# Performance work log

Measured on AMD Instinct MI355X. Metric: run time of the kernel, lower is better.

## Reference

```python
import jax, jax.numpy as jnp
import numpy as np

H, W, WS, KS, D, CF, HEAD = 64, 64, 8, 8, 512, 128, 8
INC = D + CF  # 640
GH, GW = H // WS, W // WS  # 8, 8
G = GH * GW  # 64 windows
NW = WS * WS  # 64 tokens per window
DH = D // HEAD  # 64


def _ln(x, g, b, eps=1e-5):
    m = jnp.mean(x, axis=-1, keepdims=True)
    v = jnp.var(x, axis=-1, keepdims=True)
    return (x - m) * jax.lax.rsqrt(v + eps) * g + b


def _lin(x, w, b):
    # torch Linear: w [out,in]
    return jnp.einsum('...i,oi->...o', x, w) + b


def _dwconv(x_nchw, w, b):
    # depthwise conv, stride=KS, VALID; w [C,1,KS,KS]
    y = jax.lax.conv_general_dilated(
        x_nchw, w, window_strides=(KS, KS), padding='VALID',
        feature_group_count=x_nchw.shape[1])
    return y + b[None, :, None, None]


def _win(x):  # [bt,H,W,c] -> [bt,G,NW,c]
    bt, _, _, c = x.shape
    x = x.reshape(bt, GH, WS, GW, WS, c).transpose(0, 1, 3, 2, 4, 5)
    return x.reshape(bt, G, NW, c)


def setup_inputs() -> dict:
    key = jax.random.key(0)
    ks = jax.random.split(key, 20)
    s = 0.02
    inp = {
        'x': jax.random.normal(ks[0], (8, H * W, D), jnp.float32),
        'f': jax.random.normal(ks[1], (8, H * W, CF), jnp.float32),
        'wq': jax.random.normal(ks[2], (D, INC), jnp.float32) * s,
        'bq': jnp.zeros((D,), jnp.float32),
        'wk': jax.random.normal(ks[3], (D, INC), jnp.float32) * s,
        'bk': jnp.zeros((D,), jnp.float32),
        'wv': jax.random.normal(ks[4], (D, D), jnp.float32) * s,
        'bv': jnp.zeros((D,), jnp.float32),
        'wo': jax.random.normal(ks[5], (D, D), jnp.float32) * s,
        'bo': jnp.zeros((D,), jnp.float32),
        'rw_w': jax.random.normal(ks[6], (INC, INC), jnp.float32) * s,
        'rw_b': jnp.zeros((INC,), jnp.float32),
        'convk_w': jax.random.normal(ks[7], (INC, 1, KS, KS), jnp.float32) * s,
        'convk_b': jnp.zeros((INC,), jnp.float32),
        'convv_w': jax.random.normal(ks[8], (D, 1, KS, KS), jnp.float32) * s,
        'convv_b': jnp.zeros((D,), jnp.float32),
        'qn_g': jnp.ones((INC,), jnp.float32), 'qn_b': jnp.zeros((INC,), jnp.float32),
        'kn_g': jnp.ones((INC,), jnp.float32), 'kn_b': jnp.zeros((INC,), jnp.float32),
        'vn_g': jnp.ones((D,), jnp.float32), 'vn_b': jnp.zeros((D,), jnp.float32),
        't': 1,
    }
    return inp


def reference(x, f, wq, bq, wk, bk, wv, bv, wo, bo, rw_w, rw_b,
              convk_w, convk_b, convv_w, convv_b,
              qn_g, qn_b, kn_g, kn_b, vn_g, vn_b, t):
    bt, n, c = x.shape
    x4 = x.reshape(bt, H, W, c)
    f4 = f.reshape(bt, H, W, CF)
    # no padding: H,W divisible by WS
    qk = jnp.concatenate([x4, f4], axis=-1)  # [bt,H,W,INC]
    qk = qk * jax.nn.sigmoid(_lin(qk, rw_w, rw_b))
    q = _win(qk)  # [bt,G,NW,INC]
    # global K tokens via depthwise strided conv
    kg = _dwconv(qk.transpose(0, 3, 1, 2), convk_w, convk_b)  # [bt,INC,GH,GW]
    kg = kg.transpose(0, 2, 3, 1).reshape(bt, 1, -1, INC)
    kg = jnp.broadcast_to(kg, (bt, G, kg.shape[2], INC))
    k = jnp.concatenate([q, kg], axis=2)  # [bt,G,NW+Ng,INC]
    q = _ln(q, qn_g, qn_b)
    k = _ln(k, kn_g, kn_b)
    # global V tokens
    vg = _dwconv(x4.transpose(0, 3, 1, 2), convv_w, convv_b)  # [bt,D,GH,GW]
    vg = vg.transpose(0, 2, 3, 1).reshape(bt, 1, -1, c)
    vg = jnp.broadcast_to(vg, (bt, G, vg.shape[2], c))
    xw = _win(x4)  # [bt,G,NW,c]
    v = _ln(jnp.concatenate([xw, vg], axis=2), vn_g, vn_b)
    # projections
    query = _lin(q, wq, bq).reshape(bt, G, NW, HEAD, DH)
    key = _lin(k, wk, bk).reshape(bt, G, -1, HEAD, DH)
    value = _lin(v, wv, bv).reshape(bt, G, -1, HEAD, DH)
    scores = jnp.einsum('bgqhd,bgkhd->bghqk', query, key) / jnp.sqrt(jnp.float32(DH))
    attn = jax.nn.softmax(scores, axis=-1)
    out = jnp.einsum('bghqk,bgkhd->bgqhd', attn, value).reshape(bt, G, NW, c)
    # window reverse
    out = out.reshape(bt, GH, GW, WS, WS, c).transpose(0, 1, 3, 2, 4, 5)
    out = out.reshape(bt, H * W, c)
    return _lin(out, wo, bo)
```

## Files before the change

kernel.cpp:

```cpp
#include <hip/hip_runtime.h>

typedef unsigned short u16;
typedef __attribute__((ext_vector_type(8))) short s8v;
typedef __attribute__((ext_vector_type(4))) short s4v;
typedef __attribute__((ext_vector_type(4))) float f4v;

#define NTOK 32768
#define TTOK 33280

__device__ __forceinline__ float bf2f(u16 u){
  union { unsigned int i; float f; } p; p.i = ((unsigned int)u) << 16; return p.f;
}
__device__ __forceinline__ u16 f2bf(float f){
  union { float f; unsigned int i; } p; p.f = f;
  unsigned int r = p.i + 0x7FFFu + ((p.i >> 16) & 1u);
  return (u16)(r >> 16);
}
__device__ __forceinline__ int wtok_idx(int b, int gh, int gw, int n){
  return b*4096 + (gh*8 + (n>>3))*64 + gw*8 + (n&7);
}
__device__ __forceinline__ void gload16(const u16* g, u16* l){
  __builtin_amdgcn_global_load_lds(
      (const __attribute__((address_space(1))) void*)g,
      (__attribute__((address_space(3))) void*)l, 16, 0, 0);
}

__global__ __launch_bounds__(256) void prep_weights(
    const float* __restrict__ rww, const float* __restrict__ wq,
    const float* __restrict__ wk,  const float* __restrict__ wv,
    const float* __restrict__ wo,  const float* __restrict__ qng,
    const float* __restrict__ kng, const float* __restrict__ vng,
    u16* __restrict__ orw, u16* __restrict__ oqk,
    u16* __restrict__ ov,  u16* __restrict__ oo)
{
  int i = blockIdx.x*256 + threadIdx.x;
  if (i < 409600){ orw[i] = f2bf(rww[i]); return; }
  i -= 409600;
  if (i < 327680){ oqk[i] = f2bf(wq[i] * qng[i % 640]); return; }
  i -= 327680;
  if (i < 327680){ oqk[327680 + i] = f2bf(wk[i] * kng[i % 640]); return; }
  i -= 327680;
  if (i < 262144){ ov[i] = f2bf(wv[i] * vng[i & 511]); return; }
  i -= 262144;
  oo[i] = f2bf(wo[i]);
}

__global__ __launch_bounds__(256) void prep_bias(
    const float* __restrict__ wq, const float* __restrict__ bq, const float* __restrict__ qnb,
    const float* __restrict__ qng,
    const float* __restrict__ wk, const float* __restrict__ bk, const float* __restrict__ knb,
    const float* __restrict__ kng,
    const float* __restrict__ wv, const float* __restrict__ bv, const float* __restrict__ vnb,
    const float* __restrict__ vng,
    float* __restrict__ obqk, float* __restrict__ obv,
    float* __restrict__ owsqk, float* __restrict__ owsv)
{
  int o = blockIdx.x*256 + threadIdx.x;
  int which = o >> 9;
  int oo = o & 511;
  if (which == 0){
    float s = bq[oo], ws = 0.f;
    for (int i=0;i<640;i++){ float w = wq[oo*640+i]*qng[i]; s += qnb[i]*wq[oo*640+i]; ws += w; }
    obqk[oo] = s; owsqk[oo] = ws;
  } else if (which == 1){
    float s = bk[oo], ws = 0.f;
    for (int i=0;i<640;i++){ float w = wk[oo*640+i]*kng[i]; s += knb[i]*wk[oo*640+i]; ws += w; }
    obqk[512 + oo] = s; owsqk[512 + oo] = ws;
  } else {
    float s = bv[oo], ws = 0.f;
    for (int i=0;i<512;i++){ float w = wv[oo*512+i]*vng[i]; s += vnb[i]*wv[oo*512+i]; ws += w; }
    obv[oo] = s; owsv[oo] = ws;
  }
}

__global__ __launch_bounds__(256) void build_qk(
    const float* __restrict__ X, const float* __restrict__ F, u16* __restrict__ qkb)
{
  int idx = blockIdx.x*256 + threadIdx.x;
  int token = idx / 160;
  int c4 = (idx - token*160) * 4;
  f4v v;
  if (c4 < 512) v = *(const f4v*)(X + (size_t)token*512 + c4);
  else          v = *(const f4v*)(F + (size_t)token*128 + (c4 - 512));
  s4v o;
  #pragma unroll
  for (int j=0;j<4;j++) o[j] = (short)f2bf(v[j]);
  *(s4v*)(qkb + (size_t)token*640 + c4) = o;
}

template<int NC>
__global__ __launch_bounds__(256) void row_stats(
    const u16* __restrict__ A, int stride, float* __restrict__ om, float* __restrict__ os)
{
  int t = blockIdx.x*16 + (threadIdx.x >> 4);
  int l = threadIdx.x & 15;
  const u16* row = A + (size_t)t*stride;
  float s = 0.f, s2 = 0.f;
  #pragma unroll
  for (int p=0; p<NC/128; p++){
    s8v v = *(const s8v*)(row + (p*16+l)*8);
    #pragma unroll
    for (int j=0;j<8;j++){ float x = bf2f((u16)v[j]); s += x; s2 += x*x; }
  }
  #pragma unroll
  for (int m=1;m<16;m<<=1){ s += __shfl_xor(s,m); s2 += __shfl_xor(s2,m); }
  if (l == 0){
    float mean = s*(1.f/NC);
    float var = s2*(1.f/NC) - mean*mean;
    om[t] = mean;
    os[t] = rsqrtf(var + 1e-5f);
  }
}

template<int EPI, bool STATS>
__global__ __launch_bounds__(256, 3) void gemm_kernel(
    const u16* __restrict__ A, int strideA,
    const u16* __restrict__ A2, int strideA2,
    const u16* __restrict__ B, const float* __restrict__ bias,
    const float* __restrict__ wsum,
    const float* __restrict__ rmean, const float* __restrict__ rrstd,
    u16* __restrict__ out0, u16* __restrict__ out1, float* __restrict__ outf,
    int N, int K)
{
  __shared__ u16 lA[128*64];
  __shared__ u16 lB[128*64];
  const int tid = threadIdx.x;
  const int lane = tid & 63;
  const int w = tid >> 6;
  const int wm = (w >> 1) * 64;
  const int wn = (w & 1) * 64;
  const int nb = N >> 7;
  const int nwg = (int)gridDim.x;
  const int wg = ((int)blockIdx.x & 7) * (nwg >> 3) + ((int)blockIdx.x >> 3);
  const int m0 = (wg / nb) << 7;
  const int n0 = (wg % nb) << 7;
  const int wbase = tid & ~63;

  const f4v fzero = {0.f, 0.f, 0.f, 0.f};
  f4v acc[4][4];
  #pragma unroll
  for (int i=0;i<4;i++)
    #pragma unroll
    for (int j=0;j<4;j++) acc[i][j] = fzero;

  for (int k0 = 0; k0 < K; k0 += 64){
    #pragma unroll
    for (int it=0; it<4; it++){
      int s = it*256 + tid;
      int row = s >> 3, cc = s & 7, cs = cc ^ (row & 7);
      int rr = m0 + row;
      const u16* aptr = (rr < NTOK)
          ? A  + (size_t)rr*strideA  + k0 + cs*8
          : A2 + (size_t)(rr - NTOK)*strideA2 + k0 + cs*8;
      gload16(aptr, &lA[(it*256 + wbase)*8]);
      gload16(B + (size_t)(n0+row)*K + k0 + cs*8, &lB[(it*256 + wbase)*8]);
    }
    __syncthreads();
    #pragma unroll
    for (int kk=0; kk<2; kk++){
      const int cg = kk*4 + (lane>>4);
      s8v bfr[4];
      #pragma unroll
      for (int ni=0; ni<4; ni++){
        int col = wn + ni*16 + (lane&15);
        bfr[ni] = *(const s8v*)&lB[(col*8 + (cg ^ (col&7)))*8];
      }
      #pragma unroll
      for (int mi=0; mi<4; mi++){
        int row = wm + mi*16 + (lane&15);
        s8v afr = *(const s8v*)&lA[(row*8 + (cg ^ (row&7)))*8];
        #pragma unroll
        for (int ni=0; ni<4; ni++)
          acc[mi][ni] = __builtin_amdgcn_mfma_f32_16x16x32_bf16(afr, bfr[ni], acc[mi][ni], 0, 0, 0);
      }
    }
    __syncthreads();
  }

  #pragma unroll
  for (int mi=0; mi<4; mi++){
    float rs[4], rm[4];
    if constexpr (STATS){
      #pragma unroll
      for (int j=0;j<4;j++){
        int rowg = m0 + wm + mi*16 + (lane>>4)*4 + j;
        rs[j] = rrstd[rowg]; rm[j] = rmean[rowg];
      }
    }
    #pragma unroll
    for (int ni=0; ni<4; ni++){
      const int colg = n0 + wn + ni*16 + (lane&15);
      const float bb = bias[colg];
      const float wsc = STATS ? wsum[colg] : 0.f;
      if constexpr (EPI == 3){
        const int rowg0 = m0 + wm + mi*16 + (lane>>4)*4;
        s4v pk;
        #pragma unroll
        for (int j=0;j<4;j++){
          float v = STATS ? (rs[j]*acc[mi][ni][j] - rs[j]*rm[j]*wsc + bb)
                          : (acc[mi][ni][j] + bb);
          pk[j] = (short)f2bf(v);
        }
        *(s4v*)(out0 + (size_t)colg*TTOK + rowg0) = pk;
      } else {
        #pragma unroll
        for (int j=0;j<4;j++){
          const int rowg = m0 + wm + mi*16 + (lane>>4)*4 + j;
          float v = STATS ? (rs[j]*acc[mi][ni][j] - rs[j]*rm[j]*wsc + bb)
                          : (acc[mi][ni][j] + bb);
          if constexpr (EPI == 1){
            float sg = 1.f / (1.f + __expf(-v));
            float qv = bf2f(A[(size_t)rowg*640 + colg]);
            out0[(size_t)rowg*640 + colg] = f2bf(qv * sg);
          } else if constexpr (EPI == 2){
            outf[(size_t)rowg*512 + colg] = v;
          } else {
            if (colg < 512) out0[(size_t)rowg*512 + colg] = f2bf(v);
            else            out1[(size_t)rowg*512 + (colg-512)] = f2bf(v);
          }
        }
      }
    }
  }
}

__global__ __launch_bounds__(640) void convk_ln_kernel(
    const u16* __restrict__ qkrw, const float* __restrict__ cw,
    const float* __restrict__ cb, u16* __restrict__ qkc,
    float* __restrict__ om, float* __restrict__ os)
{
  int bg = blockIdx.x;
  int b = bg >> 6, gpos = bg & 63;
  int gh = gpos >> 3, gw = gpos & 7;
  int ch = threadIdx.x;
  int base = b*4096 + gh*8*64 + gw*8;
  float acc = cb[ch];
  #pragma unroll
  for (int r=0;r<8;r++)
    #pragma unroll
    for (int c=0;c<8;c++)
      acc += bf2f(qkrw[(size_t)(base + r*64 + c)*640 + ch]) * cw[ch*64 + r*8 + c];
  float s = acc, s2 = acc*acc;
  #pragma unroll
  for (int m=1;m<64;m<<=1){ s += __shfl_xor(s,m); s2 += __shfl_xor(s2,m); }
  __shared__ float rs[10], rs2[10];
  int wid = threadIdx.x >> 6, lane = threadIdx.x & 63;
  if (lane == 0){ rs[wid] = s; rs2[wid] = s2; }
  __syncthreads();
  float ts = 0.f, ts2 = 0.f;
  #pragma unroll
  for (int i=0;i<10;i++){ ts += rs[i]; ts2 += rs2[i]; }
  float mean = ts*(1.f/640.f);
  float var = ts2*(1.f/640.f) - mean*mean;
  float rstd = rsqrtf(var + 1e-5f);
  qkc[(size_t)bg*640 + ch] = f2bf((acc-mean)*rstd);
  if (ch == 0){ om[NTOK + bg] = 0.f; os[NTOK + bg] = 1.f; }
}

__global__ __launch_bounds__(512) void convv_ln_kernel(
    const float* __restrict__ X, const float* __restrict__ cw,
    const float* __restrict__ cb, u16* __restrict__ xc,
    float* __restrict__ om, float* __restrict__ os)
{
  int bg = blockIdx.x;
  int b = bg >> 6, gpos = bg & 63;
  int gh = gpos >> 3, gw = gpos & 7;
  int ch = threadIdx.x;
  int base = b*4096 + gh*8*64 + gw*8;
  float acc = cb[ch];
  #pragma unroll
  for (int r=0;r<8;r++)
    #pragma unroll
    for (int c=0;c<8;c++)
      acc += X[(size_t)(base + r*64 + c)*512 + ch] * cw[ch*64 + r*8 + c];
  float s = acc, s2 = acc*acc;
  #pragma unroll
  for (int m=1;m<64;m<<=1){ s += __shfl_xor(s,m); s2 += __shfl_xor(s2,m); }
  __shared__ float rs[8], rs2[8];
  int wid = threadIdx.x >> 6, lane = threadIdx.x & 63;
  if (lane == 0){ rs[wid] = s; rs2[wid] = s2; }
  __syncthreads();
  float ts = 0.f, ts2 = 0.f;
  #pragma unroll
  for (int i=0;i<8;i++){ ts += rs[i]; ts2 += rs2[i]; }
  float mean = ts*(1.f/512.f);
  float var = ts2*(1.f/512.f) - mean*mean;
  float rstd = rsqrtf(var + 1e-5f);
  xc[(size_t)bg*512 + ch] = f2bf((acc-mean)*rstd);
  if (ch == 0){ om[NTOK + bg] = 0.f; os[NTOK + bg] = 1.f; }
}

__global__ __launch_bounds__(256, 3) void attn_kernel(
    const u16* __restrict__ Qp, const u16* __restrict__ Kp,
    const u16* __restrict__ VT, u16* __restrict__ Out)
{
  int blk = blockIdx.x;
  int h = blk & 7, g = (blk >> 3) & 63, b = blk >> 9;
  int gh = g >> 3, gw = g & 7;
  int tid = threadIdx.x, lane = tid & 63, wvid = tid >> 6;
  int l15 = lane & 15, lg = lane >> 4;

  __shared__ u16 ps[64*128];
  __shared__ float red[4][64];

  s8v qf[4][2], kf[2][2], vf[4];
  #pragma unroll
  for (int mi=0; mi<4; mi++){
    const u16* qrow = Qp + (size_t)wtok_idx(b,gh,gw, mi*16 + l15)*512 + h*64;
    #pragma unroll
    for (int kk=0; kk<2; kk++)
      qf[mi][kk] = *(const s8v*)(qrow + (kk*4+lg)*8);
  }
  #pragma unroll
  for (int ni=0; ni<2; ni++){
    int kt = wvid*32 + ni*16 + l15;
    int tok = (kt < 64) ? wtok_idx(b,gh,gw,kt) : (NTOK + b*64 + (kt-64));
    const u16* krow = Kp + (size_t)tok*512 + h*64;
    #pragma unroll
    for (int kk=0; kk<2; kk++)
      kf[ni][kk] = *(const s8v*)(krow + (kk*4+lg)*8);
  }
  {
    int d = wvid*16 + l15;
    const u16* vrow = VT + (size_t)(h*64 + d)*TTOK;
    #pragma unroll
    for (int c4=0; c4<4; c4++){
      int kt0 = (c4*4+lg)*8;
      int tok0 = (kt0 < 64) ? wtok_idx(b,gh,gw,kt0) : (NTOK + b*64 + (kt0-64));
      vf[c4] = *(const s8v*)(vrow + tok0);
    }
  }

  const f4v fzero = {0.f,0.f,0.f,0.f};
  f4v sacc[4][2];
  #pragma unroll
  for (int i=0;i<4;i++){ sacc[i][0]=fzero; sacc[i][1]=fzero; }
  #pragma unroll
  for (int kk=0; kk<2; kk++)
    #pragma unroll
    for (int mi=0; mi<4; mi++)
      #pragma unroll
      for (int ni=0; ni<2; ni++)
        sacc[mi][ni] = __builtin_amdgcn_mfma_f32_16x16x32_bf16(qf[mi][kk], kf[ni][kk], sacc[mi][ni], 0,0,0);

  float psum[4][4];
  #pragma unroll
  for (int mi=0; mi<4; mi++){
    #pragma unroll
    for (int j=0;j<4;j++){
      float e0 = __expf(sacc[mi][0][j] * 0.125f);
      float e1 = __expf(sacc[mi][1][j] * 0.125f);
      sacc[mi][0][j] = e0; sacc[mi][1][j] = e1;
      float t0 = e0 + e1;
      #pragma unroll
      for (int m=1;m<16;m<<=1) t0 += __shfl_xor(t0, m);
      psum[mi][j] = t0;
    }
  }
  if (l15 == 0){
    #pragma unroll
    for (int mi=0; mi<4; mi++)
      #pragma unroll
      for (int j=0;j<4;j++)
        red[wvid][mi*16 + lg*4 + j] = psum[mi][j];
  }
  __syncthreads();

  #pragma unroll
  for (int mi=0; mi<4; mi++){
    #pragma unroll
    for (int j=0;j<4;j++){
      int r = mi*16 + lg*4 + j;
      float inv = 1.0f / (red[0][r] + red[1][r] + red[2][r] + red[3][r]);
      #pragma unroll
      for (int ni=0; ni<2; ni++){
        int col = wvid*32 + ni*16 + l15;
        int ck = (col >> 3) ^ (r & 15);
        ps[r*128 + ck*8 + (col & 7)] = f2bf(sacc[mi][ni][j] * inv);
      }
    }
  }
  __syncthreads();

  f4v oacc[4];
  #pragma unroll
  for (int i=0;i<4;i++) oacc[i] = fzero;
  #pragma unroll
  for (int c4=0; c4<4; c4++){
    int cg = c4*4 + lg;
    #pragma unroll
    for (int mi=0; mi<4; mi++){
      s8v afr = *(const s8v*)&ps[((mi*16 + l15)*16 + (cg ^ l15))*8];
      oacc[mi] = __builtin_amdgcn_mfma_f32_16x16x32_bf16(afr, vf[c4], oacc[mi], 0,0,0);
    }
  }
  #pragma unroll
  for (int mi=0; mi<4; mi++)
    #pragma unroll
    for (int j=0;j<4;j++){
      int q = mi*16 + lg*4 + j;
      Out[(size_t)wtok_idx(b,gh,gw,q)*512 + h*64 + wvid*16 + l15] = f2bf(oacc[mi][j]);
    }
}

extern "C" void kernel_launch(void* const* d_in, const int* in_sizes, int n_in,
                              void* d_out, int out_size, void* d_ws, size_t ws_size,
                              hipStream_t stream)
{
  const float* X   = (const float*)d_in[0];
  const float* F   = (const float*)d_in[1];
  const float* wq  = (const float*)d_in[2];
  const float* bq  = (const float*)d_in[3];
  const float* wk  = (const float*)d_in[4];
  const float* bk  = (const float*)d_in[5];
  const float* wv  = (const float*)d_in[6];
  const float* bv  = (const float*)d_in[7];
  const float* wo  = (const float*)d_in[8];
  const float* bo  = (const float*)d_in[9];
  const float* rww = (const float*)d_in[10];
  const float* rwb = (const float*)d_in[11];
  const float* ckw = (const float*)d_in[12];
  const float* ckb = (const float*)d_in[13];
  const float* cvw = (const float*)d_in[14];
  const float* cvb = (const float*)d_in[15];
  const float* qng = (const float*)d_in[16];
  const float* qnb = (const float*)d_in[17];
  const float* kng = (const float*)d_in[18];
  const float* knb = (const float*)d_in[19];
  const float* vng = (const float*)d_in[20];
  const float* vnb = (const float*)d_in[21];
  float* OutF = (float*)d_out;

  char* ws = (char*)d_ws;
  size_t off = 0;
  auto alloc = [&](size_t bytes){
    size_t o = off; off += (bytes + 255) & ~(size_t)255; return o;
  };
  u16*   W_RW = (u16*)  (ws + alloc((size_t)640*640*2));
  u16*   W_QK = (u16*)  (ws + alloc((size_t)1024*640*2));
  u16*   W_V  = (u16*)  (ws + alloc((size_t)512*512*2));
  u16*   W_O  = (u16*)  (ws + alloc((size_t)512*512*2));
  float* B_QK = (float*)(ws + alloc(1024*4));
  float* B_V  = (float*)(ws + alloc(512*4));
  float* WS_QK= (float*)(ws + alloc(1024*4));
  float* WS_V = (float*)(ws + alloc(512*4));
  u16*   QKB  = (u16*)  (ws + alloc((size_t)NTOK*640*2));
  u16*   QKRW = (u16*)  (ws + alloc((size_t)NTOK*640*2));
  u16*   QKC  = (u16*)  (ws + alloc((size_t)512*640*2));
  u16*   XC   = (u16*)  (ws + alloc((size_t)512*512*2));
  u16*   KP   = (u16*)  (ws + alloc((size_t)TTOK*512*2));
  u16*   VT   = (u16*)  (ws + alloc((size_t)512*TTOK*2));
  float* SQm  = (float*)(ws + alloc((size_t)TTOK*4));
  float* SQs  = (float*)(ws + alloc((size_t)TTOK*4));
  float* SVm  = (float*)(ws + alloc((size_t)TTOK*4));
  float* SVs  = (float*)(ws + alloc((size_t)TTOK*4));
  (void)in_sizes; (void)n_in; (void)out_size; (void)ws_size;

  prep_weights<<<6208, 256, 0, stream>>>(rww, wq, wk, wv, wo, qng, kng, vng,
                                         W_RW, W_QK, W_V, W_O);
  prep_bias<<<6, 256, 0, stream>>>(wq, bq, qnb, qng, wk, bk, knb, kng,
                                   wv, bv, vnb, vng, B_QK, B_V, WS_QK, WS_V);
  build_qk<<<20480, 256, 0, stream>>>(X, F, QKB);

  gemm_kernel<1,false><<<1280, 256, 0, stream>>>(QKB, 640, nullptr, 0, W_RW, rwb,
      nullptr, nullptr, nullptr, QKRW, nullptr, nullptr, 640, 640);

  row_stats<640><<<2048, 256, 0, stream>>>(QKRW, 640, SQm, SQs);
  row_stats<512><<<2048, 256, 0, stream>>>(QKB, 640, SVm, SVs);
  convk_ln_kernel<<<512, 640, 0, stream>>>(QKRW, ckw, ckb, QKC, SQm, SQs);
  convv_ln_kernel<<<512, 512, 0, stream>>>(X, cvw, cvb, XC, SVm, SVs);

  gemm_kernel<3,true><<<1040, 256, 0, stream>>>(QKB, 640, XC, 512, W_V, B_V,
      WS_V, SVm, SVs, VT, nullptr, nullptr, 512, 512);
  gemm_kernel<4,true><<<2080, 256, 0, stream>>>(QKRW, 640, QKC, 640, W_QK, B_QK,
      WS_QK, SQm, SQs, QKB, KP, nullptr, 1024, 640);

  attn_kernel<<<4096, 256, 0, stream>>>(QKB, KP, VT, QKRW);

  gemm_kernel<2,false><<<1024, 256, 0, stream>>>(QKRW, 512, nullptr, 0, W_O, bo,
      nullptr, nullptr, nullptr, nullptr, nullptr, OutF, 512, 512);
}
```

Measured before the change: 456.4 us.

## Fuse row statistics into producers, merge conv-LN kernels, parallelize bias prep

The separate row_stats passes are removed. V-side LayerNorm statistics are now computed inside build_qk while X is converted to bf16. Q-side sum and sum-of-squares are accumulated with atomics in the rw GEMM's sigmoid-gating epilogue, and the QK GEMM finalizes mean and rstd from them. The two depthwise conv+LN kernels are merged into one launch, and prep_bias uses 16 lanes per output row with a shuffle reduction. GEMM launch bounds rise to 4 waves per SIMD. The aim is to avoid re-reading the QKRW and QKB activations for statistics and to cut launch count, at the cost of atomic traffic, register pressure and a variance formula that depends on float atomic ordering.

New measurement: 449.6 us. Within noise of the previous version (-1.5%).

```diff
diff --git a/kernel.cpp b/kernel.cpp
--- a/kernel.cpp
+++ b/kernel.cpp
@@ -46,79 +46,86 @@
 }
 
 __global__ __launch_bounds__(256) void prep_bias(
-    const float* __restrict__ wq, const float* __restrict__ bq, const float* __restrict__ qnb,
-    const float* __restrict__ qng,
-    const float* __restrict__ wk, const float* __restrict__ bk, const float* __restrict__ knb,
-    const float* __restrict__ kng,
-    const float* __restrict__ wv, const float* __restrict__ bv, const float* __restrict__ vnb,
-    const float* __restrict__ vng,
+    const float* __restrict__ wq, const float* __restrict__ bq,
+    const float* __restrict__ qnb, const float* __restrict__ qng,
+    const float* __restrict__ wk, const float* __restrict__ bk,
+    const float* __restrict__ knb, const float* __restrict__ kng,
+    const float* __restrict__ wv, const float* __restrict__ bv,
+    const float* __restrict__ vnb, const float* __restrict__ vng,
     float* __restrict__ obqk, float* __restrict__ obv,
     float* __restrict__ owsqk, float* __restrict__ owsv)
 {
-  int o = blockIdx.x*256 + threadIdx.x;
-  int which = o >> 9;
-  int oo = o & 511;
-  if (which == 0){
-    float s = bq[oo], ws = 0.f;
-    for (int i=0;i<640;i++){ float w = wq[oo*640+i]*qng[i]; s += qnb[i]*wq[oo*640+i]; ws += w; }
-    obqk[oo] = s; owsqk[oo] = ws;
-  } else if (which == 1){
-    float s = bk[oo], ws = 0.f;
-    for (int i=0;i<640;i++){ float w = wk[oo*640+i]*kng[i]; s += knb[i]*wk[oo*640+i]; ws += w; }
-    obqk[512 + oo] = s; owsqk[512 + oo] = ws;
-  } else {
-    float s = bv[oo], ws = 0.f;
-    for (int i=0;i<512;i++){ float w = wv[oo*512+i]*vng[i]; s += vnb[i]*wv[oo*512+i]; ws += w; }
-    obv[oo] = s; owsv[oo] = ws;
-  }
+  int o = blockIdx.x*16 + (threadIdx.x >> 4);
+  int l = threadIdx.x & 15;
+  int which = o >> 9, oo = o & 511;
+  const float *W, *LB, *LG, *BS; int KK; float *OB, *OWS; int oidx;
+  if (which == 0){ W=wq; LB=qnb; LG=qng; BS=bq; KK=640; OB=obqk; OWS=owsqk; oidx=oo; }
+  else if (which == 1){ W=wk; LB=knb; LG=kng; BS=bk; KK=640; OB=obqk; OWS=owsqk; oidx=512+oo; }
+  else { W=wv; LB=vnb; LG=vng; BS=bv; KK=512; OB=obv; OWS=owsv; oidx=oo; }
+  float s = 0.f, ws = 0.f;
+  for (int i=l; i<KK; i+=16){
+    float w = W[(size_t)oo*KK + i];
+    s += LB[i]*w;
+    ws += w*LG[i];
+  }
+  #pragma unroll
+  for (int m=1;m<16;m<<=1){ s += __shfl_xor(s,m); ws += __shfl_xor(ws,m); }
+  if (l == 0){ OB[oidx] = s + BS[oo]; OWS[oidx] = ws; }
 }
 
 __global__ __launch_bounds__(256) void build_qk(
-    const float* __restrict__ X, const float* __restrict__ F, u16* __restrict__ qkb)
-{
-  int idx = blockIdx.x*256 + threadIdx.x;
-  int token = idx / 160;
-  int c4 = (idx - token*160) * 4;
-  f4v v;
-  if (c4 < 512) v = *(const f4v*)(X + (size_t)token*512 + c4);
-  else          v = *(const f4v*)(F + (size_t)token*128 + (c4 - 512));
-  s4v o;
-  #pragma unroll
-  for (int j=0;j<4;j++) o[j] = (short)f2bf(v[j]);
-  *(s4v*)(qkb + (size_t)token*640 + c4) = o;
-}
-
-template<int NC>
-__global__ __launch_bounds__(256) void row_stats(
-    const u16* __restrict__ A, int stride, float* __restrict__ om, float* __restrict__ os)
-{
-  int t = blockIdx.x*16 + (threadIdx.x >> 4);
+    const float* __restrict__ X, const float* __restrict__ F, u16* __restrict__ qkb,
+    float* __restrict__ svm, float* __restrict__ svs,
+    float* __restrict__ sqs, float* __restrict__ sqs2)
+{
+  int blk = blockIdx.x;
+  int t = blk*16 + (threadIdx.x >> 4);
   int l = threadIdx.x & 15;
-  const u16* row = A + (size_t)t*stride;
+  const float* xrow = X + (size_t)t*512;
+  u16* orow = qkb + (size_t)t*640;
   float s = 0.f, s2 = 0.f;
   #pragma unroll
-  for (int p=0; p<NC/128; p++){
-    s8v v = *(const s8v*)(row + (p*16+l)*8);
-    #pragma unroll
-    for (int j=0;j<8;j++){ float x = bf2f((u16)v[j]); s += x; s2 += x*x; }
+  for (int p=0;p<8;p++){
+    f4v v = *(const f4v*)(xrow + (p*16+l)*4);
+    s4v ov;
+    #pragma unroll
+    for (int j=0;j<4;j++){
+      u16 r = f2bf(v[j]);
+      ov[j] = (short)r;
+      float rf = bf2f(r);
+      s += rf; s2 += rf*rf;
+    }
+    *(s4v*)(orow + (p*16+l)*4) = ov;
+  }
+  const float* frow = F + (size_t)t*128;
+  #pragma unroll
+  for (int p=0;p<2;p++){
+    f4v v = *(const f4v*)(frow + (p*16+l)*4);
+    s4v ov;
+    #pragma unroll
+    for (int j=0;j<4;j++) ov[j] = (short)f2bf(v[j]);
+    *(s4v*)(orow + 512 + (p*16+l)*4) = ov;
   }
   #pragma unroll
   for (int m=1;m<16;m<<=1){ s += __shfl_xor(s,m); s2 += __shfl_xor(s2,m); }
   if (l == 0){
-    float mean = s*(1.f/NC);
-    float var = s2*(1.f/NC) - mean*mean;
-    om[t] = mean;
-    os[t] = rsqrtf(var + 1e-5f);
-  }
-}
-
-template<int EPI, bool STATS>
-__global__ __launch_bounds__(256, 3) void gemm_kernel(
+    float mean = s*(1.f/512.f);
+    float var = s2*(1.f/512.f) - mean*mean;
+    svm[t] = mean; svs[t] = rsqrtf(var + 1e-5f);
+  }
+  int tid = threadIdx.x;
+  if (tid < 16) sqs[blk*16 + tid] = 0.f;
+  else if (tid < 32) sqs2[blk*16 + (tid-16)] = 0.f;
+}
+
+template<int EPI, int SMODE>
+__global__ __launch_bounds__(256, 4) void gemm_kernel(
     const u16* __restrict__ A, int strideA,
     const u16* __restrict__ A2, int strideA2,
     const u16* __restrict__ B, const float* __restrict__ bias,
     const float* __restrict__ wsum,
-    const float* __restrict__ rmean, const float* __restrict__ rrstd,
+    const float* __restrict__ st0, const float* __restrict__ st1,
+    float* __restrict__ sacc0, float* __restrict__ sacc1,
     u16* __restrict__ out0, u16* __restrict__ out1, float* __restrict__ outf,
     int N, int K)
 {
@@ -177,28 +184,66 @@
     __syncthreads();
   }
 
+  if constexpr (EPI == 1){
+    #pragma unroll
+    for (int mi=0; mi<4; mi++){
+      #pragma unroll
+      for (int j=0;j<4;j++){
+        const int rowg = m0 + wm + mi*16 + (lane>>4)*4 + j;
+        float t = 0.f, t2 = 0.f;
+        #pragma unroll
+        for (int ni=0; ni<4; ni++){
+          const int colg = n0 + wn + ni*16 + (lane&15);
+          float v = acc[mi][ni][j] + bias[colg];
+          float sg = 1.f / (1.f + __expf(-v));
+          float qv = bf2f(A[(size_t)rowg*640 + colg]);
+          u16 r = f2bf(qv * sg);
+          out0[(size_t)rowg*640 + colg] = r;
+          float rf = bf2f(r);
+          t += rf; t2 += rf*rf;
+        }
+        #pragma unroll
+        for (int m=1;m<16;m<<=1){ t += __shfl_xor(t,m); t2 += __shfl_xor(t2,m); }
+        if ((lane & 15) == 0){
+          atomicAdd(&sacc0[rowg], t);
+          atomicAdd(&sacc1[rowg], t2);
+        }
+      }
+    }
+    return;
+  }
+
   #pragma unroll
   for (int mi=0; mi<4; mi++){
     float rs[4], rm[4];
-    if constexpr (STATS){
+    if constexpr (SMODE == 1){
       #pragma unroll
       for (int j=0;j<4;j++){
         int rowg = m0 + wm + mi*16 + (lane>>4)*4 + j;
-        rs[j] = rrstd[rowg]; rm[j] = rmean[rowg];
+        rm[j] = st0[rowg]; rs[j] = st1[rowg];
+      }
+    } else if constexpr (SMODE == 2){
+      #pragma unroll
+      for (int j=0;j<4;j++){
+        int rowg = m0 + wm + mi*16 + (lane>>4)*4 + j;
+        float ss = st0[rowg], ss2 = st1[rowg];
+        float mean = ss*(1.f/640.f);
+        float var = ss2*(1.f/640.f) - mean*mean;
+        rm[j] = mean; rs[j] = rsqrtf(var + 1e-5f);
       }
     }
     #pragma unroll
     for (int ni=0; ni<4; ni++){
       const int colg = n0 + wn + ni*16 + (lane&15);
       const float bb = bias[colg];
-      const float wsc = STATS ? wsum[colg] : 0.f;
+      const float wsc = (SMODE != 0) ? wsum[colg] : 0.f;
       if constexpr (EPI == 3){
         const int rowg0 = m0 + wm + mi*16 + (lane>>4)*4;
         s4v pk;
         #pragma unroll
         for (int j=0;j<4;j++){
-          float v = STATS ? (rs[j]*acc[mi][ni][j] - rs[j]*rm[j]*wsc + bb)
-                          : (acc[mi][ni][j] + bb);
+          float v = (SMODE != 0) ? (rs[j]*acc[mi][ni][j] - rs[j]*rm[j]*wsc + bb)
+                                 : (acc[mi][ni][j] + bb);
           pk[j] = (short)f2bf(v);
         }
         *(s4v*)(out0 + (size_t)colg*TTOK + rowg0) = pk;
@@ -206,13 +251,9 @@
         #pragma unroll
         for (int j=0;j<4;j++){
           const int rowg = m0 + wm + mi*16 + (lane>>4)*4 + j;
-          float v = STATS ? (rs[j]*acc[mi][ni][j] - rs[j]*rm[j]*wsc + bb)
-                          : (acc[mi][ni][j] + bb);
-          if constexpr (EPI == 1){
-            float sg = 1.f / (1.f + __expf(-v));
-            float qv = bf2f(A[(size_t)rowg*640 + colg]);
-            out0[(size_t)rowg*640 + colg] = f2bf(qv * sg);
-          } else if constexpr (EPI == 2){
+          float v = (SMODE != 0) ? (rs[j]*acc[mi][ni][j] - rs[j]*rm[j]*wsc + bb)
+                                 : (acc[mi][ni][j] + bb);
+          if constexpr (EPI == 2){
             outf[(size_t)rowg*512 + colg] = v;
           } else {
             if (colg < 512) out0[(size_t)rowg*512 + colg] = f2bf(v);
@@ -224,70 +265,74 @@
   }
 }
 
-__global__ __launch_bounds__(640) void convk_ln_kernel(
-    const u16* __restrict__ qkrw, const float* __restrict__ cw,
-    const float* __restrict__ cb, u16* __restrict__ qkc,
-    float* __restrict__ om, float* __restrict__ os)
+__global__ __launch_bounds__(640) void conv_ln_kernel(
+    const u16* __restrict__ qkrw, const float* __restrict__ X,
+    const float* __restrict__ ckw, const float* __restrict__ ckb,
+    const float* __restrict__ cvw, const float* __restrict__ cvb,
+    u16* __restrict__ qkc, u16* __restrict__ xc,
+    float* __restrict__ sqs, float* __restrict__ sqs2,
+    float* __restrict__ svm, float* __restrict__ svs)
 {
   int bg = blockIdx.x;
   int b = bg >> 6, gpos = bg & 63;
   int gh = gpos >> 3, gw = gpos & 7;
   int ch = threadIdx.x;
   int base = b*4096 + gh*8*64 + gw*8;
-  float acc = cb[ch];
+
+  float acck = ckb[ch];
   #pragma unroll
   for (int r=0;r<8;r++)
     #pragma unroll
     for (int c=0;c<8;c++)
-      acc += bf2f(qkrw[(size_t)(base + r*64 + c)*640 + ch]) * cw[ch*64 + r*8 + c];
-  float s = acc, s2 = acc*acc;
-  #pragma unroll
-  for (int m=1;m<64;m<<=1){ s += __shfl_xor(s,m); s2 += __shfl_xor(s2,m); }
-  __shared__ float rs[10], rs2[10];
+      acck += bf2f(qkrw[(size_t)(base + r*64 + c)*640 + ch]) * ckw[ch*64 + r*8 + c];
+
+  float accv = 0.f;
+  if (ch < 512){
+    accv = cvb[ch];
+    #pragma unroll
+    for (int r=0;r<8;r++)
+      #pragma unroll
+      for (int c=0;c<8;c++)
+        accv += X[(size_t)(base + r*64 + c)*512 + ch] * cvw[ch*64 + r*8 + c];
+  }
+
   int wid = threadIdx.x >> 6, lane = threadIdx.x & 63;
-  if (lane == 0){ rs[wid] = s; rs2[wid] = s2; }
+  float sk = acck, sk2 = acck*acck;
+  float sv = accv, sv2 = accv*accv;
+  #pragma unroll
+  for (int m=1;m<64;m<<=1){
+    sk += __shfl_xor(sk,m); sk2 += __shfl_xor(sk2,m);
+    sv += __shfl_xor(sv,m); sv2 += __shfl_xor(sv2,m);
+  }
+  __shared__ float rk[10], rk2[10], rv[8], rv2[8];
+  if (lane == 0){
+    rk[wid] = sk; rk2[wid] = sk2;
+    if (wid < 8){ rv[wid] = sv; rv2[wid] = sv2; }
+  }
   __syncthreads();
-  float ts = 0.f, ts2 = 0.f;
-  #pragma unroll
-  for (int i=0;i<10;i++){ ts += rs[i]; ts2 += rs2[i]; }
-  float mean = ts*(1.f/640.f);
-  float var = ts2*(1.f/640.f) - mean*mean;
-  float rstd = rsqrtf(var + 1e-5f);
-  qkc[(size_t)bg*640 + ch] = f2bf((acc-mean)*rstd);
-  if (ch == 0){ om[NTOK + bg] = 0.f; os[NTOK + bg] = 1.f; }
-}
-
-__global__ __launch_bounds__(512) void convv_ln_kernel(
-    const float* __restrict__ X, const float* __restrict__ cw,
-    const float* __restrict__ cb, u16* __restrict__ xc,
-    float* __restrict__ om, float* __restrict__ os)
-{
-  int bg = blockIdx.x;
-  int b = bg >> 6, gpos = bg & 63;
-  int gh = gpos >> 3, gw = gpos & 7;
-  int ch = threadIdx.x;
-  int base = b*4096 + gh*8*64 + gw*8;
-  float acc = cb[ch];
-  #pragma unroll
-  for (int r=0;r<8;r++)
-    #pragma unroll
-    for (int c=0;c<8;c++)
-      acc += X[(size_t)(base + r*64 + c)*512 + ch] * cw[ch*64 + r*8 + c];
-  float s = acc, s2 = acc*acc;
-  #pragma unroll
-  for (int m=1;m<64;m<<=1){ s += __shfl_xor(s,m); s2 += __shfl_xor(s2,m); }
-  __shared__ float rs[8], rs2[8];
-  int wid = threadIdx.x >> 6, lane = threadIdx.x & 63;
-  if (lane == 0){ rs[wid] = s; rs2[wid] = s2; }
-  __syncthreads();
-  float ts = 0.f, ts2 = 0.f;
-  #pragma unroll
-  for (int i=0;i<8;i++){ ts += rs[i]; ts2 += rs2[i]; }
-  float mean = ts*(1.f/512.f);
-  float var = ts2*(1.f/512.f) - mean*mean;
-  float rstd = rsqrtf(var + 1e-5f);
-  xc[(size_t)bg*512 + ch] = f2bf((acc-mean)*rstd);
-  if (ch == 0){ om[NTOK + bg] = 0.f; os[NTOK + bg] = 1.f; }
+  float tk = 0.f, tk2 = 0.f;
+  #pragma unroll
+  for (int i=0;i<10;i++){ tk += rk[i]; tk2 += rk2[i]; }
+  float meank = tk*(1.f/640.f);
+  float vark = tk2*(1.f/640.f) - meank*meank;
+  float rstdk = rsqrtf(vark + 1e-5f);
+  qkc[(size_t)bg*640 + ch] = f2bf((acck-meank)*rstdk);
+
+  if (ch < 512){
+    float tv = 0.f, tv2 = 0.f;
+    #pragma unroll
+    for (int i=0;i<8;i++){ tv += rv[i]; tv2 += rv2[i]; }
+    float meanv = tv*(1.f/512.f);
+    float varv = tv2*(1.f/512.f) - meanv*meanv;
+    float rstdv = rsqrtf(varv + 1e-5f);
+    xc[(size_t)bg*512 + ch] = f2bf((accv-meanv)*rstdv);
+  }
+  if (ch == 0){
+    sqs[NTOK + bg] = 0.f;
+    sqs2[NTOK + bg] = 640.f*(1.f - 1e-5f);
+    svm[NTOK + bg] = 0.f;
+    svs[NTOK + bg] = 1.f;
+  }
 }
 
 __global__ __launch_bounds__(256, 3) void attn_kernel(
@@ -450,33 +495,31 @@
   u16*   XC   = (u16*)  (ws + alloc((size_t)512*512*2));
   u16*   KP   = (u16*)  (ws + alloc((size_t)TTOK*512*2));
   u16*   VT   = (u16*)  (ws + alloc((size_t)512*TTOK*2));
-  float* SQm  = (float*)(ws + alloc((size_t)TTOK*4));
-  float* SQs  = (float*)(ws + alloc((size_t)TTOK*4));
+  float* SQs0 = (float*)(ws + alloc((size_t)TTOK*4));
+  float* SQs1 = (float*)(ws + alloc((size_t)TTOK*4));
   float* SVm  = (float*)(ws + alloc((size_t)TTOK*4));
   float* SVs  = (float*)(ws + alloc((size_t)TTOK*4));
   (void)in_sizes; (void)n_in; (void)out_size; (void)ws_size;
 
   prep_weights<<<6208, 256, 0, stream>>>(rww, wq, wk, wv, wo, qng, kng, vng,
                                          W_RW, W_QK, W_V, W_O);
-  prep_bias<<<6, 256, 0, stream>>>(wq, bq, qnb, qng, wk, bk, knb, kng,
-                                   wv, bv, vnb, vng, B_QK, B_V, WS_QK, WS_V);
-  build_qk<<<20480, 256, 0, stream>>>(X, F, QKB);
-
-  gemm_kernel<1,false><<<1280, 256, 0, stream>>>(QKB, 640, nullptr, 0, W_RW, rwb,
-      nullptr, nullptr, nullptr, QKRW, nullptr, nullptr, 640, 640);
-
-  row_stats<640><<<2048, 256, 0, stream>>>(QKRW, 640, SQm, SQs);
-  row_stats<512><<<2048, 256, 0, stream>>>(QKB, 640, SVm, SVs);
-  convk_ln_kernel<<<512, 640, 0, stream>>>(QKRW, ckw, ckb, QKC, SQm, SQs);
-  convv_ln_kernel<<<512, 512, 0, stream>>>(X, cvw, cvb, XC, SVm, SVs);
-
-  gemm_kernel<3,true><<<1040, 256, 0, stream>>>(QKB, 640, XC, 512, W_V, B_V,
-      WS_V, SVm, SVs, VT, nullptr, nullptr, 512, 512);
-  gemm_kernel<4,true><<<2080, 256, 0, stream>>>(QKRW, 640, QKC, 640, W_QK, B_QK,
-      WS_QK, SQm, SQs, QKB, KP, nullptr, 1024, 640);
+  prep_bias<<<96, 256, 0, stream>>>(wq, bq, qnb, qng, wk, bk, knb, kng,
+                                    wv, bv, vnb, vng, B_QK, B_V, WS_QK, WS_V);
+  build_qk<<<2048, 256, 0, stream>>>(X, F, QKB, SVm, SVs, SQs0, SQs1);
+
+  gemm_kernel<1,0><<<1280, 256, 0, stream>>>(QKB, 640, nullptr, 0, W_RW, rwb,
+      nullptr, nullptr, nullptr, SQs0, SQs1, QKRW, nullptr, nullptr, 640, 640);
+
+  conv_ln_kernel<<<512, 640, 0, stream>>>(QKRW, X, ckw, ckb, cvw, cvb,
+      QKC, XC, SQs0, SQs1, SVm, SVs);
+
+  gemm_kernel<3,1><<<1040, 256, 0, stream>>>(QKB, 640, XC, 512, W_V, B_V,
+      WS_V, SVm, SVs, nullptr, nullptr, VT, nullptr, nullptr, 512, 512);
+  gemm_kernel<4,2><<<2080, 256, 0, stream>>>(QKRW, 640, QKC, 640, W_QK, B_QK,
+      WS_QK, SQs0, SQs1, nullptr, nullptr, QKB, KP, nullptr, 1024, 640);
 
   attn_kernel<<<4096, 256, 0, stream>>>(QKB, KP, VT, QKRW);
 
-  gemm_kernel<2,false><<<1024, 256, 0, stream>>>(QKRW, 512, nullptr, 0, W_O, bo,
-      nullptr, nullptr, nullptr, nullptr, nullptr, OutF, 512, 512);
-}
+  gemm_kernel<2,0><<<1024, 256, 0, stream>>>(QKRW, 512, nullptr, 0, W_O, bo,
+      nullptr, nullptr, nullptr, nullptr, nullptr, nullptr, nullptr, OutF, 512, 512);
+}
```
